# Performance work log

Hardware: AMD Instinct MI355X
Metric: run time of the kernel (lower is better)

## Reference

```python
import jax, jax.numpy as jnp
import numpy as np

B, N, D_MODEL, D_INNER = 8, 1024, 512, 2048
N_HEAD, D_K, D_V = 8, 64, 64
N_EXPERTS, TOP_K = 24, 2
N_GROUPS = 4
EPS = 1e-6


def setup_inputs() -> dict:
    key = jax.random.key(0)
    ks = jax.random.split(key, 12)
    s = 0.02
    rn = lambda k, shp: jax.random.normal(k, shp, dtype=jnp.float32) * s
    inp = {
        "x": jax.random.normal(ks[0], (B, N, D_MODEL), dtype=jnp.float32),
        "wq": rn(ks[1], (D_MODEL, N_HEAD * D_K)),
        "wk": rn(ks[2], (D_MODEL, N_HEAD * D_K)),
        "wv": rn(ks[3], (D_MODEL, N_HEAD * D_V)),
        "wo": rn(ks[4], (N_HEAD * D_V, D_MODEL)),
        "ln_attn_g": jnp.ones((D_MODEL,), jnp.float32),
        "ln_attn_b": jnp.zeros((D_MODEL,), jnp.float32),
        "wg1": rn(ks[5], (D_MODEL, N_EXPERTS)),
        "w1": rn(ks[6], (N_EXPERTS, D_MODEL, D_INNER)),
        "b1": jnp.zeros((N_EXPERTS, D_INNER), jnp.float32),
        "wg2": rn(ks[7], (D_INNER, N_EXPERTS)),
        "w2": rn(ks[8], (N_EXPERTS, D_INNER, D_MODEL)),
        "b2": jnp.zeros((N_EXPERTS, D_MODEL), jnp.float32),
        "ln_out_g": jnp.ones((D_MODEL,), jnp.float32),
        "ln_out_b": jnp.zeros((D_MODEL,), jnp.float32),
    }
    for i in range(1, 5):
        inp[f"ln{i}_g"] = jnp.ones((D_INNER,), jnp.float32)
        inp[f"ln{i}_b"] = jnp.zeros((D_INNER,), jnp.float32)
    return inp


def _ln(x, g, b):
    m = jnp.mean(x, -1, keepdims=True)
    v = jnp.mean((x - m) ** 2, -1, keepdims=True)
    return (x - m) * jax.lax.rsqrt(v + EPS) * g + b


def _gate(xf, wg, capacity):
    # top-2 gating with capacity-limited one-hot dispatch (GShard-style)
    gates = jax.nn.softmax(xf @ wg)                      # [T,E]
    w, idx = jax.lax.top_k(gates, TOP_K)                 # [T,2]
    w = w / jnp.sum(w, -1, keepdims=True)
    m1 = jax.nn.one_hot(idx[:, 0], N_EXPERTS, dtype=xf.dtype)
    m2 = jax.nn.one_hot(idx[:, 1], N_EXPERTS, dtype=xf.dtype)
    loc1 = jnp.cumsum(m1, 0) - 1.0                       # slot within expert
    loc2 = jnp.cumsum(m2, 0) - 1.0 + jnp.sum(m1, 0)[None, :]
    m1 = m1 * (loc1 < capacity)
    m2 = m2 * (loc2 < capacity)
    c1 = w[:, 0, None, None] * m1[:, :, None] * jax.nn.one_hot(loc1.astype(jnp.int32), capacity, dtype=xf.dtype)
    c2 = w[:, 1, None, None] * m2[:, :, None] * jax.nn.one_hot(loc2.astype(jnp.int32), capacity, dtype=xf.dtype)
    combine = c1 + c2                                    # [T,E,C]
    dispatch = (combine > 0).astype(xf.dtype)
    return combine, dispatch


def _moe(xf, combine, dispatch, W, b):
    ein = jnp.einsum('tec,td->ecd', dispatch, xf)        # gather into expert slots
    out = jnp.einsum('ecd,edh->ech', ein, W) + b[:, None, :]
    return jnp.einsum('tec,ech->th', combine, out)       # weighted combine


def reference(x, wq, wk, wv, wo, ln_attn_g, ln_attn_b, wg1, w1, b1, wg2, w2, b2,
              ln1_g, ln1_b, ln2_g, ln2_b, ln3_g, ln3_b, ln4_g, ln4_b,
              ln_out_g, ln_out_b):
    # ---- multi-head self-attention ----
    temp = D_K ** 0.5
    q = (x @ wq).reshape(B, N, N_HEAD, D_K)
    k = (x @ wk).reshape(B, N, N_HEAD, D_K)
    v = (x @ wv).reshape(B, N, N_HEAD, D_V)
    attn = jax.nn.softmax(jnp.einsum('bnhd,bmhd->bhnm', q / temp, k), axis=-1)
    ctx = jnp.einsum('bhnm,bmhd->bnhd', attn, v).reshape(B, N, N_HEAD * D_V)
    ctx = jax.nn.relu(ctx @ wo) + x                      # dropout is identity at eval
    ctx = _ln(ctx, ln_attn_g, ln_attn_b)
    # ---- TaskMoE positionwise FFN over 4 sequence groups ----
    resid = ctx
    xg = ctx.reshape(B, N_GROUPS, N // N_GROUPS, D_MODEL)
    T = B * (N // N_GROUPS)
    cap = int(np.ceil(T * TOP_K / N_EXPERTS))
    ln_gs = [ln1_g, ln2_g, ln3_g, ln4_g]
    ln_bs = [ln1_b, ln2_b, ln3_b, ln4_b]
    outs = []
    for i in range(N_GROUPS):
        xf = xg[:, i].reshape(T, D_MODEL)
        combine, dispatch = _gate(xf, wg1, cap)          # routing reused by 2nd MoE
        h = _moe(xf, combine, dispatch, w1, b1)          # [T, D_INNER]
        h = jax.nn.relu(_ln(h, ln_gs[i], ln_bs[i]))
        o = _moe(h, combine, dispatch, w2, b2)           # [T, D_MODEL]
        outs.append(o.reshape(B, N // N_GROUPS, D_MODEL))
    y = jnp.concatenate(outs, axis=1) + resid
    return _ln(y, ln_out_g, ln_out_b)
```

## Files before the change

### kernel.cpp

```cpp
#include <hip/hip_runtime.h>
#include <cstdint>


#define NTOK 8192
#define DM   512
#define DI   2048
#define NEXP 24
#define TPG  2048
#define CAP  171
#define CAPR 176
#define EPSF 1e-6f

typedef __bf16 bf16x8 __attribute__((ext_vector_type(8)));
typedef float f32x4 __attribute__((ext_vector_type(4)));

static __device__ __forceinline__ unsigned short f2bf(float f) {
  unsigned int u = __builtin_bit_cast(unsigned int, f);
  u = (u + 0x7fffu + ((u >> 16) & 1u)) >> 16;
  return (unsigned short)u;
}
static __device__ __forceinline__ unsigned int pk2(float a, float b) {
  return (unsigned int)f2bf(a) | ((unsigned int)f2bf(b) << 16);
}

__global__ __launch_bounds__(256) void convw(
    const float* __restrict__ in, unsigned short* __restrict__ out, int K, int N)
{
  __shared__ unsigned short T[64][65];
  int e = blockIdx.z;
  const float* ip = in + (size_t)e * K * N;
  unsigned short* op = out + (size_t)e * N * K;
  int n0 = blockIdx.x * 64, k0 = blockIdx.y * 64;
  int tid = threadIdx.x;
  #pragma unroll
  for (int i = 0; i < 16; ++i) {
    int lin = tid + i * 256;
    int k = lin >> 6, n = lin & 63;
    T[n][k] = f2bf(ip[(size_t)(k0 + k) * N + n0 + n]);
  }
  __syncthreads();
  #pragma unroll
  for (int i = 0; i < 16; ++i) {
    int lin = tid + i * 256;
    int n = lin >> 6, k = lin & 63;
    op[(size_t)(n0 + n) * K + k0 + k] = T[n][k];
  }
}

__global__ __launch_bounds__(256) void convx(
    const float* __restrict__ in, unsigned short* __restrict__ out)
{
  int i = blockIdx.x * 256 + threadIdx.x;
  float4 v = ((const float4*)in)[i];
  uint2 p;
  p.x = pk2(v.x, v.y); p.y = pk2(v.z, v.w);
  ((uint2*)out)[i] = p;
}

__global__ __launch_bounds__(256) void mfma_gemm(
    const unsigned short* __restrict__ A, int lda,
    const unsigned short* __restrict__ Bt,
    const float* __restrict__ bias,
    const int* __restrict__ lrow, const float* __restrict__ lw,
    const int* __restrict__ cnts,
    float* __restrict__ Cf, unsigned short* __restrict__ Cb,
    const float* __restrict__ Add,
    int M, int N, int K, int mode, float scale)
{
  __shared__ unsigned short As[64 * 72];
  __shared__ unsigned short Bs[128 * 72];
  int tid = threadIdx.x;
  int w = tid >> 6, lane = tid & 63, quad = lane >> 4, l16 = lane & 15;
  int n0 = blockIdx.x * 128;
  int m0 = blockIdx.y * 64;
  int pair = blockIdx.z;
  int e = pair % NEXP;
  int count = cnts ? cnts[pair] : M;
  if (m0 >= count) return;
  const int*   lr  = lrow ? lrow + pair * CAPR : nullptr;
  const float* lwp = lw   ? lw   + pair * CAPR : nullptr;

  int r8 = tid >> 3, kg = tid & 7;
  const unsigned short* aptr[2];
  #pragma unroll
  for (int i = 0; i < 2; ++i) {
    int mm = m0 + r8 + i * 32;
    if (mm >= count) mm = count - 1;
    int rm = lr ? lr[mm] : mm;
    aptr[i] = A + (size_t)rm * lda + kg * 8;
  }
  const unsigned short* Bte = Bt + (size_t)e * N * K;
  const unsigned short* bptr[4];
  #pragma unroll
  for (int i = 0; i < 4; ++i)
    bptr[i] = Bte + (size_t)(n0 + r8 + i * 32) * K + kg * 8;

  f32x4 acc[4][2] = {};
  for (int k0 = 0; k0 < K; k0 += 64) {
    __syncthreads();
    #pragma unroll
    for (int i = 0; i < 2; ++i)
      *(uint4*)&As[(r8 + i * 32) * 72 + kg * 8] = *(const uint4*)(aptr[i] + k0);
    #pragma unroll
    for (int i = 0; i < 4; ++i)
      *(uint4*)&Bs[(r8 + i * 32) * 72 + kg * 8] = *(const uint4*)(bptr[i] + k0);
    __syncthreads();
    #pragma unroll
    for (int half = 0; half < 2; ++half) {
      bf16x8 af[4];
      #pragma unroll
      for (int ms = 0; ms < 4; ++ms)
        af[ms] = *(const bf16x8*)&As[(ms * 16 + l16) * 72 + half * 32 + quad * 8];
      bf16x8 bfr[2];
      #pragma unroll
      for (int ns = 0; ns < 2; ++ns)
        bfr[ns] = *(const bf16x8*)&Bs[(w * 32 + ns * 16 + l16) * 72 + half * 32 + quad * 8];
      #pragma unroll
      for (int ms = 0; ms < 4; ++ms)
        #pragma unroll
        for (int ns = 0; ns < 2; ++ns)
          acc[ms][ns] = __builtin_amdgcn_mfma_f32_16x16x32_bf16(af[ms], bfr[ns], acc[ms][ns], 0, 0, 0);
    }
  }
  float bv[2];
  if (mode == 2) {
    #pragma unroll
    for (int ns = 0; ns < 2; ++ns)
      bv[ns] = bias[(size_t)e * N + n0 + w * 32 + ns * 16 + l16];
  }
  #pragma unroll
  for (int ms = 0; ms < 4; ++ms) {
    #pragma unroll
    for (int ns = 0; ns < 2; ++ns) {
      int col = n0 + w * 32 + ns * 16 + l16;
      #pragma unroll
      for (int r = 0; r < 4; ++r) {
        int m = m0 + ms * 16 + quad * 4 + r;
        if (mode == 0) {
          Cb[(size_t)m * N + col] = f2bf(acc[ms][ns][r] * scale);
        } else if (mode == 1) {
          Cf[(size_t)m * N + col] = fmaxf(acc[ms][ns][r], 0.f) + Add[(size_t)m * N + col];
        } else {
          if (m < count) {
            int rr = lr[m];
            float wgt = lwp[m];
            atomicAdd(&Cf[(size_t)rr * N + col], wgt * (acc[ms][ns][r] + bv[ns]));
          }
        }
      }
    }
  }
}

__global__ __launch_bounds__(256) void attn_mfma(
    const unsigned short* __restrict__ Qb, const unsigned short* __restrict__ Kb,
    const unsigned short* __restrict__ Vb, unsigned short* __restrict__ ctx)
{
  __shared__ unsigned short Ks[64 * 72];
  __shared__ unsigned short Vt[64 * 72];
  __shared__ unsigned short Ps[4][16 * 72];
  int tid = threadIdx.x;
  int w = tid >> 6, lane = tid & 63, quad = lane >> 4, l16 = lane & 15;
  int qt = blockIdx.x, bh = blockIdx.y;
  int b = bh >> 3, h = bh & 7;
  size_t hoff = (size_t)h * 64;
  size_t tokbase = (size_t)b * 1024;

  int qrow = qt * 64 + w * 16 + l16;
  const unsigned short* qp = Qb + (tokbase + qrow) * 512 + hoff + quad * 8;
  bf16x8 qa0 = *(const bf16x8*)(qp);
  bf16x8 qa1 = *(const bf16x8*)(qp + 32);

  f32x4 O[4] = {};
  float mrow[4], lrowv[4];
  #pragma unroll
  for (int r = 0; r < 4; ++r) { mrow[r] = -1e30f; lrowv[r] = 0.f; }

  for (int kv0 = 0; kv0 < 1024; kv0 += 64) {
    __syncthreads();
    {
      const unsigned short* kg = Kb + (tokbase + kv0) * 512 + hoff;
      #pragma unroll
      for (int i = 0; i < 2; ++i) {
        int f = tid + i * 256;
        int key = f >> 3, c = f & 7;
        *(uint4*)&Ks[key * 72 + c * 8] = *(const uint4*)(kg + (size_t)key * 512 + c * 8);
      }
      const unsigned short* vg = Vb + (tokbase + kv0) * 512 + hoff;
      int d = tid & 63;
      #pragma unroll
      for (int i = 0; i < 2; ++i) {
        int ko = (tid >> 6) + i * 4;
        const unsigned short* vq = vg + (size_t)ko * 8 * 512 + d;
        unsigned int a0 = vq[0],        a1 = vq[512];
        unsigned int a2 = vq[2 * 512],  a3 = vq[3 * 512];
        unsigned int a4 = vq[4 * 512],  a5 = vq[5 * 512];
        unsigned int a6 = vq[6 * 512],  a7 = vq[7 * 512];
        uint4 pk;
        pk.x = a0 | (a1 << 16); pk.y = a2 | (a3 << 16);
        pk.z = a4 | (a5 << 16); pk.w = a6 | (a7 << 16);
        *(uint4*)&Vt[d * 72 + ko * 8] = pk;
      }
    }
    __syncthreads();

    f32x4 s[4];
    #pragma unroll
    for (int kt = 0; kt < 4; ++kt) {
      const unsigned short* kr = &Ks[(kt * 16 + l16) * 72 + quad * 8];
      bf16x8 kb0 = *(const bf16x8*)(kr);
      bf16x8 kb1 = *(const bf16x8*)(kr + 32);
      f32x4 z = {};
      z = __builtin_amdgcn_mfma_f32_16x16x32_bf16(qa0, kb0, z, 0, 0, 0);
      z = __builtin_amdgcn_mfma_f32_16x16x32_bf16(qa1, kb1, z, 0, 0, 0);
      s[kt] = z;
    }

    #pragma unroll
    for (int r = 0; r < 4; ++r) {
      float mx = fmaxf(fmaxf(s[0][r], s[1][r]), fmaxf(s[2][r], s[3][r]));
      mx = fmaxf(mx, __shfl_xor(mx, 1, 64));
      mx = fmaxf(mx, __shfl_xor(mx, 2, 64));
      mx = fmaxf(mx, __shfl_xor(mx, 4, 64));
      mx = fmaxf(mx, __shfl_xor(mx, 8, 64));
      float mnew = fmaxf(mrow[r], mx);
      float alpha = __expf(mrow[r] - mnew);
      mrow[r] = mnew;
      float psum = 0.f;
      #pragma unroll
      for (int kt = 0; kt < 4; ++kt) {
        float p = __expf(s[kt][r] - mnew);
        s[kt][r] = p;
        psum += p;
      }
      psum += __shfl_xor(psum, 1, 64);
      psum += __shfl_xor(psum, 2, 64);
      psum += __shfl_xor(psum, 4, 64);
      psum += __shfl_xor(psum, 8, 64);
      lrowv[r] = lrowv[r] * alpha + psum;
      #pragma unroll
      for (int dt = 0; dt < 4; ++dt) O[dt][r] *= alpha;
    }

    #pragma unroll
    for (int kt = 0; kt < 4; ++kt)
      #pragma unroll
      for (int r = 0; r < 4; ++r)
        Ps[w][(quad * 4 + r) * 72 + kt * 16 + l16] = f2bf(s[kt][r]);
    const unsigned short* pp = &Ps[w][l16 * 72 + quad * 8];
    bf16x8 pa0 = *(const bf16x8*)(pp);
    bf16x8 pa1 = *(const bf16x8*)(pp + 32);

    #pragma unroll
    for (int dt = 0; dt < 4; ++dt) {
      const unsigned short* vr = &Vt[(dt * 16 + l16) * 72 + quad * 8];
      bf16x8 vb0 = *(const bf16x8*)(vr);
      bf16x8 vb1 = *(const bf16x8*)(vr + 32);
      O[dt] = __builtin_amdgcn_mfma_f32_16x16x32_bf16(pa0, vb0, O[dt], 0, 0, 0);
      O[dt] = __builtin_amdgcn_mfma_f32_16x16x32_bf16(pa1, vb1, O[dt], 0, 0, 0);
    }
  }

  #pragma unroll
  for (int r = 0; r < 4; ++r) {
    float inv = 1.0f / lrowv[r];
    int row = qt * 64 + w * 16 + quad * 4 + r;
    unsigned short* cp = ctx + (tokbase + row) * 512 + hoff + l16;
    #pragma unroll
    for (int dt = 0; dt < 4; ++dt) cp[dt * 16] = f2bf(O[dt][r] * inv);
  }
}

__global__ __launch_bounds__(256) void ln_kernel(
    const float* __restrict__ in, const float* __restrict__ add,
    float* __restrict__ out, unsigned short* __restrict__ outb,
    int D, int relu_after,
    const float* __restrict__ g0, const float* __restrict__ g1,
    const float* __restrict__ g2, const float* __restrict__ g3,
    const float* __restrict__ bb0, const float* __restrict__ bb1,
    const float* __restrict__ bb2, const float* __restrict__ bb3)
{
  int row = blockIdx.x;
  int grp = (row & 1023) >> 8;
  const float* g  = grp == 0 ? g0  : grp == 1 ? g1  : grp == 2 ? g2  : g3;
  const float* bb = grp == 0 ? bb0 : grp == 1 ? bb1 : grp == 2 ? bb2 : bb3;
  const float* ip = in + (size_t)row * D;
  const float* ap = add ? add + (size_t)row * D : nullptr;
  float vals[8];
  int per = D >> 8;
  float s1 = 0.f, s2 = 0.f;
  for (int i = 0; i < per; ++i) {
    int d = threadIdx.x + (i << 8);
    float vv = ip[d];
    if (ap) vv += ap[d];
    vals[i] = vv; s1 += vv; s2 += vv * vv;
  }
  #pragma unroll
  for (int o = 32; o; o >>= 1) { s1 += __shfl_xor(s1, o, 64); s2 += __shfl_xor(s2, o, 64); }
  __shared__ float sA[4], sB[4];
  int wid = threadIdx.x >> 6, lane = threadIdx.x & 63;
  if (lane == 0) { sA[wid] = s1; sB[wid] = s2; }
  __syncthreads();
  float t1 = sA[0] + sA[1] + sA[2] + sA[3];
  float t2 = sB[0] + sB[1] + sB[2] + sB[3];
  float mean = t1 / (float)D;
  float var = t2 / (float)D - mean * mean;
  float rs = rsqrtf(var + EPSF);
  float* op = out ? out + (size_t)row * D : nullptr;
  unsigned short* obp = outb ? outb + (size_t)row * D : nullptr;
  for (int i = 0; i < per; ++i) {
    int d = threadIdx.x + (i << 8);
    float o = (vals[i] - mean) * rs * g[d] + bb[d];
    if (relu_after) o = fmaxf(o, 0.f);
    if (op)  op[d] = o;
    if (obp) obp[d] = f2bf(o);
  }
}

__global__ __launch_bounds__(256) void gate1(
    const float* __restrict__ xln, const float* __restrict__ wg,
    int* __restrict__ idx0, int* __restrict__ idx1,
    float* __restrict__ w0o, float* __restrict__ w1o)
{
  int wid = threadIdx.x >> 6, lane = threadIdx.x & 63;
  int tk = blockIdx.x * 4 + wid;
  int g = tk >> 11, t = tk & 2047;
  int b = t >> 8, j = t & 255;
  size_t row = (size_t)b * 1024 + g * 256 + j;
  const float* xp = xln + row * 512;
  float acc = -1e30f;
  if (lane < 24) {
    acc = 0.f;
    for (int d = 0; d < 512; ++d) acc += xp[d] * wg[d * 24 + lane];
  }
  float b0v = -1e30f, b1v = -1e30f; int i0 = 0, i1 = 0;
  for (int e = 0; e < 24; ++e) {
    float vv = __shfl(acc, e, 64);
    if (vv > b0v)      { b1v = b0v; i1 = i0; b0v = vv; i0 = e; }
    else if (vv > b1v) { b1v = vv; i1 = e; }
  }
  if (lane == 0) {
    float w0 = 1.0f / (1.0f + __expf(b1v - b0v));
    idx0[tk] = i0; idx1[tk] = i1; w0o[tk] = w0; w1o[tk] = 1.0f - w0;
  }
}

__global__ __launch_bounds__(64) void gate2(
    const int* __restrict__ idx0, const int* __restrict__ idx1,
    const float* __restrict__ w0, const float* __restrict__ w1,
    int* __restrict__ lrow, float* __restrict__ lw, int* __restrict__ counts)
{
  int pair = blockIdx.x; int g = pair / 24; int e = pair % 24;
  int lane = threadIdx.x;
  int base = g * TPG;
  unsigned long long lm = (lane == 63) ? 0x7fffffffffffffffULL : ((1ULL << lane) - 1ULL);
  int run = 0;
  for (int it = 0; it < TPG / 64; ++it) {
    int t = it * 64 + lane;
    bool m = (idx0[base + t] == e);
    unsigned long long mask = __ballot(m);
    int pre = __popcll(mask & lm);
    int rank = run + pre;
    if (m && rank < CAP) {
      int bq = t >> 8, j = t & 255;
      lrow[pair * CAPR + rank] = bq * 1024 + g * 256 + j;
      lw[pair * CAPR + rank] = w0[base + t];
    }
    run += __popcll(mask);
  }
  int total1 = run;
  int run2 = 0;
  for (int it = 0; it < TPG / 64; ++it) {
    int t = it * 64 + lane;
    bool m = (idx1[base + t] == e);
    unsigned long long mask = __ballot(m);
    int pre = __popcll(mask & lm);
    int rank2 = run2 + pre;
    if (m && (total1 + rank2) < CAP) {
      int bq = t >> 8, j = t & 255;
      lrow[pair * CAPR + total1 + rank2] = bq * 1024 + g * 256 + j;
      lw[pair * CAPR + total1 + rank2] = w1[base + t];
    }
    run2 += __popcll(mask);
  }
  if (lane == 0) {
    int c1 = total1 < CAP ? total1 : CAP;
    int room = CAP - total1; if (room < 0) room = 0;
    int c2 = run2 < room ? run2 : room;
    counts[pair] = c1 + c2;
  }
}

extern "C" void kernel_launch(void* const* d_in, const int* in_sizes, int n_in,
                              void* d_out, int out_size, void* d_ws, size_t ws_size,
                              hipStream_t stream)
{
  const float* x   = (const float*)d_in[0];
  const float* wq  = (const float*)d_in[1];
  const float* wk  = (const float*)d_in[2];
  const float* wv  = (const float*)d_in[3];
  const float* wo  = (const float*)d_in[4];
  const float* ln_attn_g = (const float*)d_in[5];
  const float* ln_attn_b = (const float*)d_in[6];
  const float* wg1 = (const float*)d_in[7];
  const float* w1  = (const float*)d_in[8];
  const float* b1  = (const float*)d_in[9];
  const float* w2  = (const float*)d_in[11];
  const float* b2  = (const float*)d_in[12];
  const float* ln_out_g = (const float*)d_in[13];
  const float* ln_out_b = (const float*)d_in[14];
  const float* ln1g = (const float*)d_in[15]; const float* ln1b = (const float*)d_in[16];
  const float* ln2g = (const float*)d_in[17]; const float* ln2b = (const float*)d_in[18];
  const float* ln3g = (const float*)d_in[19]; const float* ln3b = (const float*)d_in[20];
  const float* ln4g = (const float*)d_in[21]; const float* ln4b = (const float*)d_in[22];

  char* ws = (char*)d_ws;
  const size_t MB = 1048576;
  unsigned short* wt1  = (unsigned short*)(ws + 0);
  unsigned short* wtq  = (unsigned short*)(ws + 48 * MB);
  unsigned short* wtk  = (unsigned short*)(ws + 48 * MB + 524288);
  unsigned short* wtv  = (unsigned short*)(ws + 49 * MB);
  unsigned short* wto  = (unsigned short*)(ws + 49 * MB + 524288);
  unsigned short* xbf  = (unsigned short*)(ws + 50 * MB);
  unsigned short* hb2  = (unsigned short*)(ws + 50 * MB);
  unsigned short* qbf  = (unsigned short*)(ws + 58 * MB);
  unsigned short* kbf  = (unsigned short*)(ws + 66 * MB);
  unsigned short* vbf  = (unsigned short*)(ws + 74 * MB);
  unsigned short* ctxb = (unsigned short*)(ws + 82 * MB);
  float* y0    = (float*)(ws + 90 * MB);
  float* ymoe  = (float*)(ws + 90 * MB);
  float* ctxln = (float*)(ws + 106 * MB);
  unsigned short* ctxlnb = (unsigned short*)(ws + 122 * MB);
  float* hb    = (float*)(ws + 130 * MB);
  unsigned short* wt2 = (unsigned short*)(ws + 130 * MB);
  char*  small = ws + 194 * MB;
  int*   idx0  = (int*)(small + 0);
  int*   idx1  = (int*)(small + 32768);
  float* w0a   = (float*)(small + 65536);
  float* w1a   = (float*)(small + 98304);
  int*   lrowp = (int*)(small + 131072);
  float* lwv   = (float*)(small + 198656);
  int*   cnts  = (int*)(small + 266240);

  dim3 blk(256);
  convw<<<dim3(8, 8, 1), blk, 0, stream>>>(wq, wtq, 512, 512);
  convw<<<dim3(8, 8, 1), blk, 0, stream>>>(wk, wtk, 512, 512);
  convw<<<dim3(8, 8, 1), blk, 0, stream>>>(wv, wtv, 512, 512);
  convw<<<dim3(8, 8, 1), blk, 0, stream>>>(wo, wto, 512, 512);
  convw<<<dim3(32, 8, 24), blk, 0, stream>>>(w1, wt1, 512, 2048);
  convx<<<4096, blk, 0, stream>>>(x, xbf);
  mfma_gemm<<<dim3(4, 128, 1), blk, 0, stream>>>(xbf, DM, wtq, nullptr, nullptr, nullptr, nullptr,
      nullptr, qbf, nullptr, NTOK, DM, DM, 0, 0.125f);
  mfma_gemm<<<dim3(4, 128, 1), blk, 0, stream>>>(xbf, DM, wtk, nullptr, nullptr, nullptr, nullptr,
      nullptr, kbf, nullptr, NTOK, DM, DM, 0, 1.0f);
  mfma_gemm<<<dim3(4, 128, 1), blk, 0, stream>>>(xbf, DM, wtv, nullptr, nullptr, nullptr, nullptr,
      nullptr, vbf, nullptr, NTOK, DM, DM, 0, 1.0f);
  attn_mfma<<<dim3(16, 64), blk, 0, stream>>>(qbf, kbf, vbf, ctxb);
  mfma_gemm<<<dim3(4, 128, 1), blk, 0, stream>>>(ctxb, DM, wto, nullptr, nullptr, nullptr, nullptr,
      y0, nullptr, x, NTOK, DM, DM, 1, 1.0f);
  ln_kernel<<<8192, blk, 0, stream>>>(y0, nullptr, ctxln, ctxlnb, DM, 0,
      ln_attn_g, ln_attn_g, ln_attn_g, ln_attn_g, ln_attn_b, ln_attn_b, ln_attn_b, ln_attn_b);
  gate1<<<2048, blk, 0, stream>>>(ctxln, wg1, idx0, idx1, w0a, w1a);
  gate2<<<96, 64, 0, stream>>>(idx0, idx1, w0a, w1a, lrowp, lwv, cnts);
  hipMemsetAsync(hb, 0, (size_t)NTOK * DI * 4, stream);
  hipMemsetAsync(ymoe, 0, (size_t)NTOK * DM * 4, stream);
  mfma_gemm<<<dim3(16, 3, 96), blk, 0, stream>>>(ctxlnb, DM, wt1, b1, lrowp, lwv, cnts,
      hb, nullptr, nullptr, 0, DI, DM, 2, 1.0f);
  ln_kernel<<<8192, blk, 0, stream>>>(hb, nullptr, nullptr, hb2, DI, 1,
      ln1g, ln2g, ln3g, ln4g, ln1b, ln2b, ln3b, ln4b);
  convw<<<dim3(8, 32, 24), blk, 0, stream>>>(w2, wt2, 2048, 512);
  mfma_gemm<<<dim3(4, 3, 96), blk, 0, stream>>>(hb2, DI, wt2, b2, lrowp, lwv, cnts,
      ymoe, nullptr, nullptr, 0, DM, DI, 2, 1.0f);
  ln_kernel<<<8192, blk, 0, stream>>>(ymoe, ctxln, (float*)d_out, nullptr, DM, 0,
      ln_out_g, ln_out_g, ln_out_g, ln_out_g, ln_out_b, ln_out_b, ln_out_b, ln_out_b);
}
```

Before: 823.9 us.

## Double-buffer GEMM tiles with direct global-to-LDS loads and XOR swizzle

The MFMA GEMM now loads A and B tiles straight into shared memory with global_load_lds, into two buffers, so the next K-tile is fetched while the current one is multiplied. The padded LDS layout is replaced by an unpadded one with an XOR swizzle on the 16-byte column group to avoid bank conflicts. This removes the register round-trip and one barrier per iteration. In exchange it doubles LDS use, which may lower occupancy, and it depends on the correctness of the swizzle and the vmcnt wait.

```diff
diff --git a/kernel.cpp b/kernel.cpp
--- a/kernel.cpp
+++ b/kernel.cpp
@@ -21,6 +21,12 @@
 }
 static __device__ __forceinline__ unsigned int pk2(float a, float b) {
   return (unsigned int)f2bf(a) | ((unsigned int)f2bf(b) << 16);
+}
+
+static __device__ __forceinline__ void gload16(const unsigned short* g, unsigned short* l) {
+  __builtin_amdgcn_global_load_lds(
+      (const __attribute__((address_space(1))) void*)g,
+      (__attribute__((address_space(3))) void*)l, 16, 0, 0);
 }
 
 __global__ __launch_bounds__(256) void convw(
@@ -67,8 +73,8 @@
     const float* __restrict__ Add,
     int M, int N, int K, int mode, float scale)
 {
-  __shared__ unsigned short As[64 * 72];
-  __shared__ unsigned short Bs[128 * 72];
+  __shared__ unsigned short As[2][64 * 64];
+  __shared__ unsigned short Bs[2][128 * 64];
   int tid = threadIdx.x;
   int w = tid >> 6, lane = tid & 63, quad = lane >> 4, l16 = lane & 15;
   int n0 = blockIdx.x * 128;
@@ -80,41 +86,57 @@
   const int*   lr  = lrow ? lrow + pair * CAPR : nullptr;
   const float* lwp = lw   ? lw   + pair * CAPR : nullptr;
 
-  int r8 = tid >> 3, kg = tid & 7;
-  const unsigned short* aptr[2];
+  int sub = lane >> 3;
+  int gsw = (lane & 7) ^ sub;
+  const unsigned short* aSrc[2];
   #pragma unroll
   for (int i = 0; i < 2; ++i) {
-    int mm = m0 + r8 + i * 32;
+    int mm = m0 + i * 32 + w * 8 + sub;
     if (mm >= count) mm = count - 1;
     int rm = lr ? lr[mm] : mm;
-    aptr[i] = A + (size_t)rm * lda + kg * 8;
+    aSrc[i] = A + (size_t)rm * lda + gsw * 8;
   }
   const unsigned short* Bte = Bt + (size_t)e * N * K;
-  const unsigned short* bptr[4];
+  const unsigned short* bSrc[4];
   #pragma unroll
   for (int i = 0; i < 4; ++i)
-    bptr[i] = Bte + (size_t)(n0 + r8 + i * 32) * K + kg * 8;
+    bSrc[i] = Bte + (size_t)(n0 + i * 32 + w * 8 + sub) * K + gsw * 8;
+
+  int wbase = w * 512;
 
   f32x4 acc[4][2] = {};
-  for (int k0 = 0; k0 < K; k0 += 64) {
+  int nt = K >> 6;
+
+  #pragma unroll
+  for (int i = 0; i < 2; ++i) gload16(aSrc[i], &As[0][i * 2048 + wbase]);
+  #pragma unroll
+  for (int i = 0; i < 4; ++i) gload16(bSrc[i], &Bs[0][i * 2048 + wbase]);
+
+  for (int t = 0; t < nt; ++t) {
+    asm volatile("s_waitcnt vmcnt(0)" ::: "memory");
     __syncthreads();
-    #pragma unroll
-    for (int i = 0; i < 2; ++i)
-      *(uint4*)&As[(r8 + i * 32) * 72 + kg * 8] = *(const uint4*)(aptr[i] + k0);
-    #pragma unroll
-    for (int i = 0; i < 4; ++i)
-      *(uint4*)&Bs[(r8 + i * 32) * 72 + kg * 8] = *(const uint4*)(bptr[i] + k0);
-    __syncthreads();
+    int cur = t & 1;
+    if (t + 1 < nt) {
+      int koff = (t + 1) << 6;
+      int nxt = cur ^ 1;
+      #pragma unroll
+      for (int i = 0; i < 2; ++i) gload16(aSrc[i] + koff, &As[nxt][i * 2048 + wbase]);
+      #pragma unroll
+      for (int i = 0; i < 4; ++i) gload16(bSrc[i] + koff, &Bs[nxt][i * 2048 + wbase]);
+    }
+    const unsigned short* Ab = As[cur];
+    const unsigned short* Bb = Bs[cur];
     #pragma unroll
     for (int half = 0; half < 2; ++half) {
+      int g8 = ((half * 4 + quad) ^ (l16 & 7)) * 8;
       bf16x8 af[4];
       #pragma unroll
       for (int ms = 0; ms < 4; ++ms)
-        af[ms] = *(const bf16x8*)&As[(ms * 16 + l16) * 72 + half * 32 + quad * 8];
+        af[ms] = *(const bf16x8*)&Ab[(ms * 16 + l16) * 64 + g8];
       bf16x8 bfr[2];
       #pragma unroll
       for (int ns = 0; ns < 2; ++ns)
-        bfr[ns] = *(const bf16x8*)&Bs[(w * 32 + ns * 16 + l16) * 72 + half * 32 + quad * 8];
+        bfr[ns] = *(const bf16x8*)&Bb[(w * 32 + ns * 16 + l16) * 64 + g8];
       #pragma unroll
       for (int ms = 0; ms < 4; ++ms)
         #pragma unroll
```

Result: no change. 829.8 us (+0.7%).
